# Kernel optimization log

Hardware: AMD Instinct MI355X
Metric: run time of the kernel (lower is better)

## Reference

```python
import jax, jax.numpy as jnp
import numpy as np

ALPHA = 0.2          # LeakyReLU negative slope
NEG = -9e15          # masking value from the torch source


def _gat_multihead(x, adj, W, a):
    """All nheads GATLayers (concat=True math, elu applied by caller).
    x: [B,N,F], adj: [B,N,N], W: [H,F,O], a: [H,2O]. Returns [B,H,N,O].
    Note a_input @ a decomposes as h_i.a[:O] + h_j.a[O:], so we never
    materialize the O(N^2 * 2O) pairwise concat tensor."""
    h = jnp.einsum('bnf,hfo->bhno', x, W)            # [B,H,N,O]
    O = h.shape[-1]
    s1 = jnp.einsum('bhno,ho->bhn', h, a[:, :O])     # h_i . a_src
    s2 = jnp.einsum('bhno,ho->bhn', h, a[:, O:])     # h_j . a_dst
    e = jax.nn.leaky_relu(s1[..., :, None] + s2[..., None, :], ALPHA)  # [B,H,N,N]
    att = jax.nn.softmax(jnp.where(adj[:, None] > 0, e, NEG), axis=-1)
    return jnp.einsum('bhij,bhjo->bhio', att, h)


def _gat_single(x, adj, W, a):
    """out_att GATLayer (concat=False, no elu). W: [F,O], a: [2O]."""
    h = jnp.einsum('bnf,fo->bno', x, W)
    O = W.shape[-1]
    s1 = h @ a[:O]
    s2 = h @ a[O:]
    e = jax.nn.leaky_relu(s1[:, :, None] + s2[:, None, :], ALPHA)
    att = jax.nn.softmax(jnp.where(adj > 0, e, NEG), axis=-1)
    return jnp.einsum('bij,bjo->bio', att, h)


def setup_inputs() -> dict:
    key = jax.random.key(0)
    ks = jax.random.split(key, 10)
    B, N, F = 2, 2048, 768
    H, O = 8, 256
    x = jax.random.normal(ks[0], (B, N, F), dtype=jnp.float32)
    # sparse-ish binary adjacency (adj>0 is all that matters) + self loops
    adj = (jax.random.uniform(ks[1], (B, N, N)) < 0.05).astype(jnp.float32)
    adj = jnp.maximum(adj, jnp.eye(N, dtype=jnp.float32)[None])
    mask = jnp.ones((B, N, 1), dtype=jnp.float32)  # unused by GAT.forward
    s = 0.05
    W_heads = jax.random.normal(ks[2], (H, F, O), dtype=jnp.float32) * s
    a_heads = jax.random.normal(ks[3], (H, 2 * O), dtype=jnp.float32) * s
    W_out = jax.random.normal(ks[4], (H * O, O), dtype=jnp.float32) * s
    a_out = jax.random.normal(ks[5], (2 * O,), dtype=jnp.float32) * s
    W_lin = jax.random.normal(ks[6], (O, H * O), dtype=jnp.float32) * s  # nn.Linear weight [out,in]
    b_lin = jnp.zeros((O,), dtype=jnp.float32)
    W_ln = jax.random.normal(ks[7], (O, O), dtype=jnp.float32) * s
    b_ln = jnp.zeros((O,), dtype=jnp.float32)
    return {"x": x, "adj": adj, "mask": mask, "W_heads": W_heads,
            "a_heads": a_heads, "W_out": W_out, "a_out": a_out,
            "W_lin": W_lin, "b_lin": b_lin, "W_ln": W_ln, "b_ln": b_ln}


def reference(x, adj, mask, W_heads, a_heads, W_out, a_out, W_lin, b_lin, W_ln, b_ln):
    # layer 0: multi-head GAT, elu, concat over heads (dropout=0 in eval)
    hp = jax.nn.elu(_gat_multihead(x, adj, W_heads, a_heads))  # [B,H,N,O]
    B, H, N, O = hp.shape
    x1 = jnp.transpose(hp, (0, 2, 1, 3)).reshape(B, N, H * O)
    # layer 1: residual linear + out_att (concat=False)
    x2 = x1 @ W_lin.T + b_lin + _gat_single(x1, adj, W_out, a_out)
    # final: relu(ln(x))
    return jax.nn.relu(x2 @ W_ln.T + b_ln)
```

## Files before the change

kernel.cpp:

```cpp
#include <hip/hip_runtime.h>
#include <hip/hip_bf16.h>

constexpr int Bb = 2, Nn = 2048, Ff = 768, Hh = 8, Oo = 256;

typedef __attribute__((ext_vector_type(8)))  short   short8;
typedef __attribute__((ext_vector_type(16))) float   f32x16;
typedef __attribute__((ext_vector_type(4)))  unsigned short ushort4_t;

__device__ inline unsigned short f2bf(float f) {
    unsigned u = __float_as_uint(f);
    u = (u + 0x7FFFu + ((u >> 16) & 1u)) >> 16;
    return (unsigned short)u;
}

__device__ inline void wfrag_kn_body(
        const float* __restrict__ W, unsigned short* __restrict__ out,
        int K, int N, int fblk, int t) {
    int f = fblk * 4 + (t >> 6);
    int slot = t & 63, kh = slot >> 5, lm = slot & 31;
    int nfk = K >> 4;
    int nt = f / nfk, kt = f - nt * nfk;
    const float* wp = W + (size_t)(kt * 16 + kh * 8) * N + nt * 32 + lm;
    ushort4_t o0, o1;
    o0.x = f2bf(wp[0]);             o0.y = f2bf(wp[(size_t)N]);
    o0.z = f2bf(wp[2 * (size_t)N]); o0.w = f2bf(wp[3 * (size_t)N]);
    o1.x = f2bf(wp[4 * (size_t)N]); o1.y = f2bf(wp[5 * (size_t)N]);
    o1.z = f2bf(wp[6 * (size_t)N]); o1.w = f2bf(wp[7 * (size_t)N]);
    unsigned short* op = out + (size_t)f * 512 + slot * 8;
    *(ushort4_t*)op = o0;
    *(ushort4_t*)(op + 4) = o1;
}

__device__ inline void wfrag_nk_body(
        const float* __restrict__ W, unsigned short* __restrict__ out,
        int K, int fblk, int t) {
    int f = fblk * 4 + (t >> 6);
    int slot = t & 63, kh = slot >> 5, lm = slot & 31;
    int nfk = K >> 4;
    int nt = f / nfk, kt = f - nt * nfk;
    const float* wp = W + (size_t)(nt * 32 + lm) * K + kt * 16 + kh * 8;
    float4 a = *(const float4*)wp, b = *(const float4*)(wp + 4);
    ushort4_t o0, o1;
    o0.x = f2bf(a.x); o0.y = f2bf(a.y); o0.z = f2bf(a.z); o0.w = f2bf(a.w);
    o1.x = f2bf(b.x); o1.y = f2bf(b.y); o1.z = f2bf(b.z); o1.w = f2bf(b.w);
    unsigned short* op = out + (size_t)f * 512 + slot * 8;
    *(ushort4_t*)op = o0;
    *(ushort4_t*)(op + 4) = o1;
}

__global__ __launch_bounds__(256) void prep_misc_kernel(
        const float* __restrict__ adj, unsigned long long* __restrict__ bits,
        const float* __restrict__ x, unsigned short* __restrict__ x_bf,
        const float* __restrict__ W_heads, unsigned short* __restrict__ WhF,
        const float* __restrict__ W_out,   unsigned short* __restrict__ WoF,
        const float* __restrict__ W_lin,   unsigned short* __restrict__ WlF,
        const float* __restrict__ W_ln,    unsigned short* __restrict__ WnF) {
    int blk = blockIdx.x, t = threadIdx.x;
    if (blk < 32768) {
        size_t gid = (size_t)blk * 256 + t;
        float v = adj[gid];
        unsigned long long m = __ballot(v > 0.f);
        if ((t & 63) == 0) bits[gid >> 6] = m;
    } else if (blk < 35840) {
        size_t i = (size_t)(blk - 32768) * 256 + t;
        float4 v = ((const float4*)x)[i];
        ushort4_t o;
        o.x = f2bf(v.x); o.y = f2bf(v.y); o.z = f2bf(v.z); o.w = f2bf(v.w);
        ((ushort4_t*)x_bf)[i] = o;
    } else if (blk < 36608) {
        int idx = blk - 35840;
        int head = idx / 96, fblk = idx - head * 96;
        wfrag_kn_body(W_heads + (size_t)head * Ff * Oo, WhF + (size_t)head * 384 * 512,
                      Ff, Oo, fblk, t);
    } else if (blk < 36864) {
        wfrag_kn_body(W_out, WoF, Hh * Oo, Oo, blk - 36608, t);
    } else if (blk < 37120) {
        wfrag_nk_body(W_lin, WlF, Hh * Oo, blk - 36864, t);
    } else {
        wfrag_nk_body(W_ln, WnF, Oo, blk - 37120, t);
    }
}

template<int SWAPZ>
__global__ __launch_bounds__(256) void gemm32_kernel(
        const unsigned short* __restrict__ A, int K, long long sA, int bAshift,
        const unsigned short* __restrict__ BF, long long sB, int bmask,
        float* __restrict__ C, long long sC,
        unsigned short* __restrict__ CF, long long sCF, int Mtot,
        const float* __restrict__ bias, int mode,
        const float* __restrict__ aall, int amask,
        float* __restrict__ E1p, float* __restrict__ E1n, float2* __restrict__ E2pn) {
    int z  = SWAPZ ? blockIdx.x : blockIdx.z;
    int mx = SWAPZ ? blockIdx.y : blockIdx.x;
    A  += (size_t)(z >> bAshift) * sA;
    BF += (size_t)(z & bmask) * sB;
    if (C) C += (size_t)z * sC;
    if (CF) CF += (size_t)z * sCF;
    int m0 = mx * 32;
    int t = threadIdx.x;
    int wv = t >> 6, lane = t & 63;
    int lm = lane & 31, kh = lane >> 5;
    int nfk = K >> 4;
    __shared__ __align__(16) unsigned short As[32][136];
    f32x16 acc[2] = {};
    int sr = t >> 3, sc2 = (t & 7) * 16;
    const unsigned short* ag  = A + (size_t)(m0 + sr) * K + sc2;
    const unsigned short* bg0 = BF + (size_t)(wv * 2) * nfk * 512;
    const unsigned short* bg1 = bg0 + (size_t)nfk * 512;
    for (int k0 = 0; k0 < K; k0 += 128) {
        *(short8*)&As[sr][sc2]     = *(const short8*)(ag + k0);
        *(short8*)&As[sr][sc2 + 8] = *(const short8*)(ag + k0 + 8);
        int kt0 = k0 >> 4;
        __syncthreads();
#pragma unroll
        for (int s = 0; s < 8; ++s) {
            short8 a0 = *(const short8*)&As[lm][s * 16 + kh * 8];
            short8 b0 = *(const short8*)(bg0 + (size_t)(kt0 + s) * 512 + lane * 8);
            short8 b1 = *(const short8*)(bg1 + (size_t)(kt0 + s) * 512 + lane * 8);
            acc[0] = __builtin_amdgcn_mfma_f32_32x32x16_bf16(a0, b0, acc[0], 0, 0, 0);
            acc[1] = __builtin_amdgcn_mfma_f32_32x32x16_bf16(a0, b1, acc[1], 0, 0, 0);
        }
        __syncthreads();
    }
#pragma unroll
    for (int nt = 0; nt < 2; ++nt) {
        int colg = wv * 64 + nt * 32 + lm;
        float bv = (mode == 2) ? bias[colg] : 0.f;
        if (C) {
#pragma unroll
            for (int reg = 0; reg < 16; ++reg) {
                int rl = 4 * kh + (reg & 3) + 8 * (reg >> 2);
                float v = acc[nt][reg];
                if (mode == 2) { v += bv; v = fmaxf(v, 0.f); }
                C[(size_t)(m0 + rl) * 256 + colg] = v;
            }
        }
        if (mode == 1) {
#pragma unroll
            for (int q = 0; q < 4; ++q) {
                int kt = m0 / 16 + (q >> 1);
                size_t fi = ((size_t)(colg >> 5) * (Mtot / 16) + kt) * 512 +
                            ((q & 1) * 32 + (colg & 31)) * 8 + kh * 4;
                ushort4_t pk;
                pk.x = f2bf(acc[nt][q * 4 + 0]);
                pk.y = f2bf(acc[nt][q * 4 + 1]);
                pk.z = f2bf(acc[nt][q * 4 + 2]);
                pk.w = f2bf(acc[nt][q * 4 + 3]);
                *(ushort4_t*)(CF + fi) = pk;
            }
        }
    }
    if (aall) {
        const float* av = aall + (size_t)(z & amask) * 512;
        float a1v0 = av[wv * 64 + lm],       a1v1 = av[wv * 64 + 32 + lm];
        float a2v0 = av[256 + wv * 64 + lm], a2v1 = av[256 + wv * 64 + 32 + lm];
        float* sbuf = (float*)As;
#pragma unroll
        for (int reg = 0; reg < 16; ++reg) {
            int rl = 4 * kh + (reg & 3) + 8 * (reg >> 2);
            float v1 = acc[0][reg] * a1v0 + acc[1][reg] * a1v1;
            float v2 = acc[0][reg] * a2v0 + acc[1][reg] * a2v1;
#pragma unroll
            for (int m = 1; m <= 16; m <<= 1) {
                v1 += __shfl_xor(v1, m, 64);
                v2 += __shfl_xor(v2, m, 64);
            }
            if (lm == 0) { sbuf[rl * 8 + wv] = v1; sbuf[rl * 8 + 4 + wv] = v2; }
        }
        __syncthreads();
        if (t < 32) {
            float s1 = sbuf[t * 8] + sbuf[t * 8 + 1] + sbuf[t * 8 + 2] + sbuf[t * 8 + 3];
            float s2 = sbuf[t * 8 + 4] + sbuf[t * 8 + 5] + sbuf[t * 8 + 6] + sbuf[t * 8 + 7];
            size_t ei = (size_t)z * Nn + m0 + t;
            E1p[ei] = __expf(s1);
            E1n[ei] = __expf(0.2f * s1);
            E2pn[ei] = make_float2(__expf(s2), __expf(0.2f * s2));
        }
    }
}

__global__ __launch_bounds__(512) void gemm32_dual_kernel(
        const unsigned short* __restrict__ A, int K, long long sA,
        const unsigned short* __restrict__ BF,
        unsigned short* __restrict__ h2f, float* __restrict__ lin,
        const float* __restrict__ a_out,
        float* __restrict__ E1p, float* __restrict__ E1n, float2* __restrict__ E2pn) {
    int b = blockIdx.z, ng = blockIdx.y;
    A += (size_t)b * sA;
    int nfk = K >> 4;
    BF += (size_t)ng * 8 * nfk * 512;
    int m0 = blockIdx.x * 32;
    int t = threadIdx.x;
    int wv = t >> 6, lane = t & 63;
    int lm = lane & 31, kh = lane >> 5;
    __shared__ __align__(16) unsigned short As[32][136];
    f32x16 acc = {};
    int sr = t >> 4, sc2 = (t & 15) * 8;
    const unsigned short* ag = A + (size_t)(m0 + sr) * K + sc2;
    const unsigned short* bg = BF + (size_t)wv * nfk * 512;
    for (int k0 = 0; k0 < K; k0 += 128) {
        *(short8*)&As[sr][sc2] = *(const short8*)(ag + k0);
        int kt0 = k0 >> 4;
        __syncthreads();
#pragma unroll
        for (int s = 0; s < 8; ++s) {
            short8 a0 = *(const short8*)&As[lm][s * 16 + kh * 8];
            short8 b0 = *(const short8*)(bg + (size_t)(kt0 + s) * 512 + lane * 8);
            acc = __builtin_amdgcn_mfma_f32_32x32x16_bf16(a0, b0, acc, 0, 0, 0);
        }
        __syncthreads();
    }
    int colg = wv * 32 + lm;
    if (ng == 1) {
        float* C = lin + (size_t)b * Nn * 256;
#pragma unroll
        for (int reg = 0; reg < 16; ++reg) {
            int rl = 4 * kh + (reg & 3) + 8 * (reg >> 2);
            C[(size_t)(m0 + rl) * 256 + colg] = acc[reg];
        }
    } else {
        unsigned short* CF = h2f + (size_t)b * 524288;
#pragma unroll
        for (int q = 0; q < 4; ++q) {
            int kt = m0 / 16 + (q >> 1);
            size_t fi = ((size_t)(colg >> 5) * 128 + kt) * 512 +
                        ((q & 1) * 32 + (colg & 31)) * 8 + kh * 4;
            ushort4_t pk;
            pk.x = f2bf(acc[q * 4 + 0]);
            pk.y = f2bf(acc[q * 4 + 1]);
            pk.z = f2bf(acc[q * 4 + 2]);
            pk.w = f2bf(acc[q * 4 + 3]);
            *(ushort4_t*)(CF + fi) = pk;
        }
        float a1v = a_out[colg];
        float a2v = a_out[256 + colg];
        float* sbuf = (float*)As;
#pragma unroll
        for (int reg = 0; reg < 16; ++reg) {
            int rl = 4 * kh + (reg & 3) + 8 * (reg >> 2);
            float v1 = acc[reg] * a1v;
            float v2 = acc[reg] * a2v;
#pragma unroll
            for (int m = 1; m <= 16; m <<= 1) {
                v1 += __shfl_xor(v1, m, 64);
                v2 += __shfl_xor(v2, m, 64);
            }
            if (lm == 0) { sbuf[rl * 16 + wv] = v1; sbuf[rl * 16 + 8 + wv] = v2; }
        }
        __syncthreads();
        if (t < 32) {
            float s1 = 0.f, s2 = 0.f;
#pragma unroll
            for (int k = 0; k < 8; ++k) {
                s1 += sbuf[t * 16 + k];
                s2 += sbuf[t * 16 + 8 + k];
            }
            size_t ei = (size_t)b * Nn + m0 + t;
            E1p[ei] = __expf(s1);
            E1n[ei] = __expf(0.2f * s1);
            E2pn[ei] = make_float2(__expf(s2), __expf(0.2f * s2));
        }
    }
}

__global__ __launch_bounds__(256) void gemm32_final_kernel(
        const float* __restrict__ pacc, const float* __restrict__ plsum,
        const float* __restrict__ lin, const float* __restrict__ b_lin,
        const unsigned short* __restrict__ BF, const float* __restrict__ b_ln,
        float* __restrict__ out) {
    int b = blockIdx.z, oc = blockIdx.y;
    int m0 = blockIdx.x * 32;
    int t = threadIdx.x;
    int wv = t >> 6, lane = t & 63;
    int lm = lane & 31, kh = lane >> 5;
    constexpr int nfk = 16;
    __shared__ __align__(16) unsigned short As[32][136];
    f32x16 acc = {};
    int sr = t >> 3, sc2 = (t & 7) * 16;
    int row = m0 + sr;
    int BN = Bb * Nn;
    size_t prow = (size_t)b * Nn + row;
    float li = 1.f / (plsum[prow] + plsum[prow + BN] + plsum[prow + 2 * BN] + plsum[prow + 3 * BN]);
    size_t ps4 = (size_t)Bb * Nn * 256;
    const unsigned short* bg = BF + (size_t)(oc * 4 + wv) * nfk * 512;
    for (int k0 = 0; k0 < 256; k0 += 128) {
        int o = k0 + sc2;
        size_t pidx = prow * 256 + o;
#pragma unroll
        for (int g = 0; g < 4; ++g) {
            float4 s4 = *(const float4*)(pacc + pidx + 4 * g);
#pragma unroll
            for (int k = 1; k < 4; ++k) {
                float4 q = *(const float4*)(pacc + k * ps4 + pidx + 4 * g);
                s4.x += q.x; s4.y += q.y; s4.z += q.z; s4.w += q.w;
            }
            float4 lv = *(const float4*)(lin + pidx + 4 * g);
            float4 bv = *(const float4*)(b_lin + o + 4 * g);
            ushort4_t pk;
            pk.x = f2bf(s4.x * li + lv.x + bv.x);
            pk.y = f2bf(s4.y * li + lv.y + bv.y);
            pk.z = f2bf(s4.z * li + lv.z + bv.z);
            pk.w = f2bf(s4.w * li + lv.w + bv.w);
            *(ushort4_t*)&As[sr][sc2 + 4 * g] = pk;
        }
        int kt0 = k0 >> 4;
        __syncthreads();
#pragma unroll
        for (int s = 0; s < 8; ++s) {
            short8 a0 = *(const short8*)&As[lm][s * 16 + kh * 8];
            short8 b0 = *(const short8*)(bg + (size_t)(kt0 + s) * 512 + lane * 8);
            acc = __builtin_amdgcn_mfma_f32_32x32x16_bf16(a0, b0, acc, 0, 0, 0);
        }
        __syncthreads();
    }
    float* C = out + (size_t)b * Nn * 256;
    int colg = oc * 128 + wv * 32 + lm;
    float bv = b_ln[colg];
#pragma unroll
    for (int reg = 0; reg < 16; ++reg) {
        int rl = 4 * kh + (reg & 3) + 8 * (reg >> 2);
        float v = fmaxf(acc[reg] + bv, 0.f);
        C[(size_t)(m0 + rl) * 256 + colg] = v;
    }
}

template<int JLEN, int MODE, int SWAPXY>
__global__ __launch_bounds__(256, 4) void attn32_kernel(
        const unsigned short* __restrict__ hfrag,
        const unsigned* __restrict__ bits,
        const float* __restrict__ E1p, const float* __restrict__ E1n,
        const float2* __restrict__ E2pn,
        unsigned short* __restrict__ outbf, int ldo,
        float* __restrict__ pacc, float* __restrict__ plsum,
        int hshift) {
    constexpr int W = JLEN / 32, NC = JLEN / 64, ABS = W + 1;
    int it = SWAPXY ? blockIdx.y : blockIdx.x;
    int bh = SWAPXY ? blockIdx.x : blockIdx.y;
    int js = blockIdx.z;
    int b = bh >> hshift, hd = bh & ((1 << hshift) - 1);
    int i0 = it * 32, jbase = js * JLEN;
    int kt0 = js * (JLEN / 16);
    int t = threadIdx.x, lane = t & 63;
    int wv = t >> 6, lm = lane & 31, kh = lane >> 5;
    int ti = t & 31, jq = t >> 5;

    __shared__ unsigned ab[32 * ABS];
    __shared__ __align__(16) unsigned short ps[2][32][64];
    __shared__ float lred[32][9];
    __shared__ float linv[32];

    const unsigned* bb = bits + ((size_t)b * Nn + i0) * 64 + (jbase >> 5);
    for (int k = t; k < 32 * W; k += 256) {
        int r = k / W, w0 = k - r * W;
        ab[r * ABS + w0] = bb[(size_t)r * 64 + w0];
    }
    __syncthreads();

    float e1p = E1p[(size_t)bh * Nn + i0 + ti];
    float e1n = E1n[(size_t)bh * Nn + i0 + ti];
    const float4* e2base = (const float4*)(E2pn + (size_t)bh * Nn + jbase);

    const unsigned short* bg0 = hfrag + (size_t)bh * 524288 + (size_t)(wv * 2) * 128 * 512;
    const unsigned short* bg1 = bg0 + 128 * 512;

    f32x16 acc[2] = {};
    float lp0 = 0.f, lp1 = 0.f;
    short8 Bpp[4][2];

    auto loadBs = [&](int c, int s, int slot) {
        int kt = kt0 + c * 4 + s;
        Bpp[slot][0] = *(const short8*)(bg0 + (size_t)kt * 512 + lane * 8);
        Bpp[slot][1] = *(const short8*)(bg1 + (size_t)kt * 512 + lane * 8);
    };
    auto computeP = [&](int c, int buf) {
        int cj = c * 64;
        unsigned word = ab[ti * ABS + (cj >> 5) + (jq >> 2)];
        unsigned field = (word >> ((jq & 3) * 8)) & 0xffu;
        const float4* ep = e2base + ((cj + jq * 8) >> 1);
        unsigned pk[4];
#pragma unroll
        for (int u = 0; u < 4; ++u) {
            float4 q = ep[u];
            float p0 = fmaxf(e1p * q.x, e1n * q.y);
            p0 = ((field >> (2 * u)) & 1u) ? p0 : 0.f;
            float p1 = fmaxf(e1p * q.z, e1n * q.w);
            p1 = ((field >> (2 * u + 1)) & 1u) ? p1 : 0.f;
            if (u & 1) lp1 += p0 + p1; else lp0 += p0 + p1;
            __hip_bfloat162 hv = __float22bfloat162_rn(make_float2(p0, p1));
            pk[u] = *(unsigned*)&hv;
        }
        uint4 v; v.x = pk[0]; v.y = pk[1]; v.z = pk[2]; v.w = pk[3];
        *(uint4*)&ps[buf][ti][(jq ^ (ti & 7)) * 8] = v;
    };
    auto mfmaS = [&](int buf, int s, int slot) {
        int g = 2 * s + kh;
        short8 a0 = *(const short8*)&ps[buf][lm][(g ^ (lm & 7)) * 8];
        __builtin_amdgcn_s_setprio(1);
        acc[0] = __builtin_amdgcn_mfma_f32_32x32x16_bf16(a0, Bpp[slot][0], acc[0], 0, 0, 0);
        acc[1] = __builtin_amdgcn_mfma_f32_32x32x16_bf16(a0, Bpp[slot][1], acc[1], 0, 0, 0);
        __builtin_amdgcn_s_setprio(0);
    };

    computeP(0, 0);
    loadBs(0, 0, 0); loadBs(0, 1, 1); loadBs(0, 2, 2); loadBs(0, 3, 3);
    __syncthreads();
    for (int c = 0; c + 1 < NC; ++c) {
        int cb = c & 1, nb = cb ^ 1;
        computeP(c + 1, nb);
        mfmaS(cb, 0, 0);  loadBs(c + 1, 0, 0);
        mfmaS(cb, 1, 1);  loadBs(c + 1, 1, 1);
        mfmaS(cb, 2, 2);  loadBs(c + 1, 2, 2);
        mfmaS(cb, 3, 3);  loadBs(c + 1, 3, 3);
        __syncthreads();
    }
    {
        int cb = (NC - 1) & 1;
        mfmaS(cb, 0, 0);
        mfmaS(cb, 1, 1);
        mfmaS(cb, 2, 2);
        mfmaS(cb, 3, 3);
    }

    lred[ti][jq] = lp0 + lp1;
    __syncthreads();
    if (MODE == 0) {
        if (t < 32) {
            float s = 0.f;
#pragma unroll
            for (int k = 0; k < 8; ++k) s += lred[t][k];
            linv[t] = 1.f / s;
        }
        __syncthreads();
#pragma unroll
        for (int nt = 0; nt < 2; ++nt) {
            int o = wv * 64 + nt * 32 + lm;
#pragma unroll
            for (int reg = 0; reg < 16; ++reg) {
                int rl = 4 * kh + (reg & 3) + 8 * (reg >> 2);
                float v = acc[nt][reg] * linv[rl];
                v = v > 0.f ? v : expm1f(v);
                outbf[((size_t)b * Nn + i0 + rl) * ldo + (size_t)hd * Oo + o] = f2bf(v);
            }
        }
    } else {
        if (t < 32) {
            float s = 0.f;
#pragma unroll
            for (int k = 0; k < 8; ++k) s += lred[t][k];
            plsum[((size_t)js * Bb + b) * Nn + i0 + t] = s;
        }
        float* pa = pacc + (((size_t)js * Bb + b) * Nn) * 256;
#pragma unroll
        for (int nt = 0; nt < 2; ++nt) {
            int o = wv * 64 + nt * 32 + lm;
#pragma unroll
            for (int reg = 0; reg < 16; ++reg) {
                int rl = 4 * kh + (reg & 3) + 8 * (reg >> 2);
                pa[(size_t)(i0 + rl) * 256 + o] = acc[nt][reg];
            }
        }
    }
}

template<int JLEN, int MODE, int SWAPXY>
__global__ __launch_bounds__(256, 2) void attn64_kernel(
        const unsigned short* __restrict__ hfrag,
        const unsigned* __restrict__ bits,
        const float* __restrict__ E1p, const float* __restrict__ E1n,
        const float2* __restrict__ E2pn,
        unsigned short* __restrict__ outbf, int ldo,
        float* __restrict__ pacc, float* __restrict__ plsum,
        int hshift) {
    constexpr int W = JLEN / 32, NC = JLEN / 64, ABS = W + 1;
    int it = SWAPXY ? blockIdx.y : blockIdx.x;
    int bh = SWAPXY ? blockIdx.x : blockIdx.y;
    int js = blockIdx.z;
    int b = bh >> hshift, hd = bh & ((1 << hshift) - 1);
    int i0 = it * 64, jbase = js * JLEN;
    int kt0 = js * (JLEN / 16);
    int t = threadIdx.x, lane = t & 63;
    int wv = t >> 6, lm = lane & 31, kh = lane >> 5;
    int ti = t & 31, jq = t >> 5;

    __shared__ unsigned ab[64 * ABS];
    __shared__ __align__(16) unsigned short ps[2][64][64];
    __shared__ float lred[64][9];
    __shared__ float linv[64];

    const unsigned* bb = bits + ((size_t)b * Nn + i0) * 64 + (jbase >> 5);
    for (int k = t; k < 64 * W; k += 256) {
        int r = k / W, w0 = k - r * W;
        ab[r * ABS + w0] = bb[(size_t)r * 64 + w0];
    }
    __syncthreads();

    float e1pA = E1p[(size_t)bh * Nn + i0 + ti];
    float e1nA = E1n[(size_t)bh * Nn + i0 + ti];
    float e1pB = E1p[(size_t)bh * Nn + i0 + 32 + ti];
    float e1nB = E1n[(size_t)bh * Nn + i0 + 32 + ti];
    const float4* e2base = (const float4*)(E2pn + (size_t)bh * Nn + jbase);

    const unsigned short* bg0 = hfrag + (size_t)bh * 524288 + (size_t)(wv * 2) * 128 * 512;
    const unsigned short* bg1 = bg0 + 128 * 512;

    f32x16 acc[4] = {};
    float lpA = 0.f, lpB = 0.f;
    short8 Bpp[4][2];

    auto loadBs = [&](int c, int s, int slot) {
        int kt = kt0 + c * 4 + s;
        Bpp[slot][0] = *(const short8*)(bg0 + (size_t)kt * 512 + lane * 8);
        Bpp[slot][1] = *(const short8*)(bg1 + (size_t)kt * 512 + lane * 8);
    };
    auto computeP = [&](int c, int buf) {
        int cj = c * 64;
        int wi = (cj >> 5) + (jq >> 2);
        unsigned wordA = ab[ti * ABS + wi];
        unsigned wordB = ab[(ti + 32) * ABS + wi];
        unsigned fieldA = (wordA >> ((jq & 3) * 8)) & 0xffu;
        unsigned fieldB = (wordB >> ((jq & 3) * 8)) & 0xffu;
        const float4* ep = e2base + ((cj + jq * 8) >> 1);
        unsigned pkA[4], pkB[4];
#pragma unroll
        for (int u = 0; u < 4; ++u) {
            float4 q = ep[u];
            float a0v = fmaxf(e1pA * q.x, e1nA * q.y);
            a0v = ((fieldA >> (2 * u)) & 1u) ? a0v : 0.f;
            float a1v = fmaxf(e1pA * q.z, e1nA * q.w);
            a1v = ((fieldA >> (2 * u + 1)) & 1u) ? a1v : 0.f;
            lpA += a0v + a1v;
            float b0v = fmaxf(e1pB * q.x, e1nB * q.y);
            b0v = ((fieldB >> (2 * u)) & 1u) ? b0v : 0.f;
            float b1v = fmaxf(e1pB * q.z, e1nB * q.w);
            b1v = ((fieldB >> (2 * u + 1)) & 1u) ? b1v : 0.f;
            lpB += b0v + b1v;
            __hip_bfloat162 hA = __float22bfloat162_rn(make_float2(a0v, a1v));
            __hip_bfloat162 hB = __float22bfloat162_rn(make_float2(b0v, b1v));
            pkA[u] = *(unsigned*)&hA;
            pkB[u] = *(unsigned*)&hB;
        }
        int col = (jq ^ (ti & 7)) * 8;
        uint4 vA; vA.x = pkA[0]; vA.y = pkA[1]; vA.z = pkA[2]; vA.w = pkA[3];
        uint4 vB; vB.x = pkB[0]; vB.y = pkB[1]; vB.z = pkB[2]; vB.w = pkB[3];
        *(uint4*)&ps[buf][ti][col] = vA;
        *(uint4*)&ps[buf][ti + 32][col] = vB;
    };
    auto mfmaS = [&](int buf, int s, int slot) {
        int g = 2 * s + kh;
        int col = (g ^ (lm & 7)) * 8;
        short8 a0 = *(const short8*)&ps[buf][lm][col];
        short8 a1 = *(const short8*)&ps[buf][32 + lm][col];
        __builtin_amdgcn_s_setprio(1);
        acc[0] = __builtin_amdgcn_mfma_f32_32x32x16_bf16(a0, Bpp[slot][0], acc[0], 0, 0, 0);
        acc[1] = __builtin_amdgcn_mfma_f32_32x32x16_bf16(a0, Bpp[slot][1], acc[1], 0, 0, 0);
        acc[2] = __builtin_amdgcn_mfma_f32_32x32x16_bf16(a1, Bpp[slot][0], acc[2], 0, 0, 0);
        acc[3] = __builtin_amdgcn_mfma_f32_32x32x16_bf16(a1, Bpp[slot][1], acc[3], 0, 0, 0);
        __builtin_amdgcn_s_setprio(0);
    };

    computeP(0, 0);
    loadBs(0, 0, 0); loadBs(0, 1, 1); loadBs(0, 2, 2); loadBs(0, 3, 3);
    __syncthreads();
    for (int c = 0; c + 1 < NC; ++c) {
        int cb = c & 1, nb = cb ^ 1;
        computeP(c + 1, nb);
        mfmaS(cb, 0, 0);  loadBs(c + 1, 0, 0);
        mfmaS(cb, 1, 1);  loadBs(c + 1, 1, 1);
        mfmaS(cb, 2, 2);  loadBs(c + 1, 2, 2);
        mfmaS(cb, 3, 3);  loadBs(c + 1, 3, 3);
        __syncthreads();
    }
    {
        int cb = (NC - 1) & 1;
        mfmaS(cb, 0, 0);
        mfmaS(cb, 1, 1);
        mfmaS(cb, 2, 2);
        mfmaS(cb, 3, 3);
    }

    lred[ti][jq] = lpA;
    lred[ti + 32][jq] = lpB;
    __syncthreads();
    if (MODE == 0) {
        if (t < 64) {
            float s = 0.f;
#pragma unroll
            for (int k = 0; k < 8; ++k) s += lred[t][k];
            linv[t] = 1.f / s;
        }
        __syncthreads();
#pragma unroll
        for (int ih = 0; ih < 2; ++ih) {
#pragma unroll
            for (int nt = 0; nt < 2; ++nt) {
                int o = wv * 64 + nt * 32 + lm;
#pragma unroll
                for (int reg = 0; reg < 16; ++reg) {
                    int rl = 4 * kh + (reg & 3) + 8 * (reg >> 2);
                    int row = ih * 32 + rl;
                    float v = acc[ih * 2 + nt][reg] * linv[row];
                    v = v > 0.f ? v : expm1f(v);
                    outbf[((size_t)b * Nn + i0 + row) * ldo + (size_t)hd * Oo + o] = f2bf(v);
                }
            }
        }
    } else {
        if (t < 64) {
            float s = 0.f;
#pragma unroll
            for (int k = 0; k < 8; ++k) s += lred[t][k];
            plsum[((size_t)js * Bb + b) * Nn + i0 + t] = s;
        }
        float* pa = pacc + (((size_t)js * Bb + b) * Nn) * 256;
#pragma unroll
        for (int ih = 0; ih < 2; ++ih) {
#pragma unroll
            for (int nt = 0; nt < 2; ++nt) {
                int o = wv * 64 + nt * 32 + lm;
#pragma unroll
                for (int reg = 0; reg < 16; ++reg) {
                    int rl = 4 * kh + (reg & 3) + 8 * (reg >> 2);
                    int row = ih * 32 + rl;
                    pa[(size_t)(i0 + row) * 256 + o] = acc[ih * 2 + nt][reg];
                }
            }
        }
    }
}

extern "C" void kernel_launch(void* const* d_in, const int* in_sizes, int n_in,
                              void* d_out, int out_size, void* d_ws, size_t ws_size,
                              hipStream_t stream) {
    const float* x       = (const float*)d_in[0];
    const float* adj     = (const float*)d_in[1];
    const float* W_heads = (const float*)d_in[3];
    const float* a_heads = (const float*)d_in[4];
    const float* W_out   = (const float*)d_in[5];
    const float* a_out   = (const float*)d_in[6];
    const float* W_lin   = (const float*)d_in[7];
    const float* b_lin   = (const float*)d_in[8];
    const float* W_ln    = (const float*)d_in[9];
    const float* b_ln    = (const float*)d_in[10];

    char* w = (char*)d_ws;
    float* pacc     = (float*)(w);
    float* lin      = (float*)(w + 33554432);
    float* E1p_mh   = (float*)(w + 41943040);
    float* E1n_mh   = (float*)(w + 42074112);
    float2* E2pn_mh = (float2*)(w + 42205184);
    float* E1p_sh   = (float*)(w + 42467328);
    float* E1n_sh   = (float*)(w + 42483712);
    float2* E2pn_sh = (float2*)(w + 42500096);
    unsigned long long* bits = (unsigned long long*)(w + 42532864);
    unsigned short* x_bf  = (unsigned short*)(w + 43581440);
    unsigned short* WhF   = (unsigned short*)(w + 49872896);
    unsigned short* WoF   = (unsigned short*)(w + 53018624);
    unsigned short* WlF   = (unsigned short*)(w + 54067200);
    unsigned short* WnF   = (unsigned short*)(w + 55115776);
    unsigned short* hfrag = (unsigned short*)(w + 55246848);
    unsigned short* h2frag= (unsigned short*)(w + 72024064);
    unsigned short* x1_bf = (unsigned short*)(w + 74121216);
    float* plsum = E1p_mh;

    prep_misc_kernel<<<37152, 256, 0, stream>>>(
        adj, bits, x, x_bf, W_heads, WhF, W_out, WoF, W_lin, WlF, W_ln, WnF);

    gemm32_kernel<1><<<dim3(Bb * Hh, Nn / 32, 1), 256, 0, stream>>>(
        x_bf, Ff, (long long)Nn * Ff, 3, WhF, 384LL * 512, 7,
        nullptr, 0, hfrag, 524288, Nn, nullptr, 1,
        a_heads, 7, E1p_mh, E1n_mh, E2pn_mh);
    attn64_kernel<2048, 0, 1><<<dim3(Bb * Hh, Nn / 64, 1), 256, 0, stream>>>(
        hfrag, (const unsigned*)bits, E1p_mh, E1n_mh, E2pn_mh,
        x1_bf, Hh * Oo, nullptr, nullptr, 3);
    gemm32_dual_kernel<<<dim3(Nn / 32, 2, Bb), 512, 0, stream>>>(
        x1_bf, Hh * Oo, (long long)Nn * Hh * Oo, WoF, h2frag, lin,
        a_out, E1p_sh, E1n_sh, E2pn_sh);
    attn32_kernel<512, 1, 0><<<dim3(Nn / 32, Bb, 4), 256, 0, stream>>>(
        h2frag, (const unsigned*)bits, E1p_sh, E1n_sh, E2pn_sh,
        nullptr, 0, pacc, plsum, 0);
    gemm32_final_kernel<<<dim3(Nn / 32, 2, Bb), 256, 0, stream>>>(
        pacc, plsum, lin, b_lin, WnF, b_ln, (float*)d_out);
}
```

Measured before the change: 237.0 us.

## Widen head GEMM to 64-row tiles and split second attention eightfold

```diff
diff --git a/kernel.cpp b/kernel.cpp
--- a/kernel.cpp
+++ b/kernel.cpp
@@ -2,6 +2,7 @@
 #include <hip/hip_bf16.h>
 
 constexpr int Bb = 2, Nn = 2048, Ff = 768, Hh = 8, Oo = 256;
+constexpr int NSPLIT = 8;
 
 typedef __attribute__((ext_vector_type(8)))  short   short8;
 typedef __attribute__((ext_vector_type(16))) float   f32x16;
@@ -81,101 +82,95 @@
     }
 }
 
-template<int SWAPZ>
-__global__ __launch_bounds__(256) void gemm32_kernel(
+__global__ __launch_bounds__(256) void gemm64_kernel(
         const unsigned short* __restrict__ A, int K, long long sA, int bAshift,
         const unsigned short* __restrict__ BF, long long sB, int bmask,
-        float* __restrict__ C, long long sC,
         unsigned short* __restrict__ CF, long long sCF, int Mtot,
-        const float* __restrict__ bias, int mode,
         const float* __restrict__ aall, int amask,
         float* __restrict__ E1p, float* __restrict__ E1n, float2* __restrict__ E2pn) {
-    int z  = SWAPZ ? blockIdx.x : blockIdx.z;
-    int mx = SWAPZ ? blockIdx.y : blockIdx.x;
+    int z  = blockIdx.x;
+    int mx = blockIdx.y;
     A  += (size_t)(z >> bAshift) * sA;
     BF += (size_t)(z & bmask) * sB;
-    if (C) C += (size_t)z * sC;
-    if (CF) CF += (size_t)z * sCF;
-    int m0 = mx * 32;
+    CF += (size_t)z * sCF;
+    int m0 = mx * 64;
     int t = threadIdx.x;
     int wv = t >> 6, lane = t & 63;
     int lm = lane & 31, kh = lane >> 5;
     int nfk = K >> 4;
-    __shared__ __align__(16) unsigned short As[32][136];
-    f32x16 acc[2] = {};
-    int sr = t >> 3, sc2 = (t & 7) * 16;
+    __shared__ __align__(16) unsigned short As[64][136];
+    f32x16 acc[4] = {};
+    int sr = t >> 2, sc2 = (t & 3) * 32;
     const unsigned short* ag  = A + (size_t)(m0 + sr) * K + sc2;
     const unsigned short* bg0 = BF + (size_t)(wv * 2) * nfk * 512;
     const unsigned short* bg1 = bg0 + (size_t)nfk * 512;
     for (int k0 = 0; k0 < K; k0 += 128) {
-        *(short8*)&As[sr][sc2]     = *(const short8*)(ag + k0);
-        *(short8*)&As[sr][sc2 + 8] = *(const short8*)(ag + k0 + 8);
+        *(short8*)&As[sr][sc2]      = *(const short8*)(ag + k0);
+        *(short8*)&As[sr][sc2 + 8]  = *(const short8*)(ag + k0 + 8);
+        *(short8*)&As[sr][sc2 + 16] = *(const short8*)(ag + k0 + 16);
+        *(short8*)&As[sr][sc2 + 24] = *(const short8*)(ag + k0 + 24);
         int kt0 = k0 >> 4;
         __syncthreads();
 #pragma unroll
         for (int s = 0; s < 8; ++s) {
             short8 a0 = *(const short8*)&As[lm][s * 16 + kh * 8];
+            short8 a1 = *(const short8*)&As[32 + lm][s * 16 + kh * 8];
             short8 b0 = *(const short8*)(bg0 + (size_t)(kt0 + s) * 512 + lane * 8);
             short8 b1 = *(const short8*)(bg1 + (size_t)(kt0 + s) * 512 + lane * 8);
             acc[0] = __builtin_amdgcn_mfma_f32_32x32x16_bf16(a0, b0, acc[0], 0, 0, 0);
             acc[1] = __builtin_amdgcn_mfma_f32_32x32x16_bf16(a0, b1, acc[1], 0, 0, 0);
-        }
-        __syncthreads();
-    }
-#pragma unroll
-    for (int nt = 0; nt < 2; ++nt) {
-        int colg = wv * 64 + nt * 32 + lm;
-        float bv = (mode == 2) ? bias[colg] : 0.f;
-        if (C) {
-#pragma unroll
-            for (int reg = 0; reg < 16; ++reg) {
-                int rl = 4 * kh + (reg & 3) + 8 * (reg >> 2);
-                float v = acc[nt][reg];
-                if (mode == 2) { v += bv; v = fmaxf(v, 0.f); }
-                C[(size_t)(m0 + rl) * 256 + colg] = v;
-            }
-        }
-        if (mode == 1) {
+            acc[2] = __builtin_amdgcn_mfma_f32_32x32x16_bf16(a1, b0, acc[2], 0, 0, 0);
+            acc[3] = __builtin_amdgcn_mfma_f32_32x32x16_bf16(a1, b1, acc[3], 0, 0, 0);
+        }
+        __syncthreads();
+    }
+#pragma unroll
+    for (int hf = 0; hf < 2; ++hf) {
+#pragma unroll
+        for (int nt = 0; nt < 2; ++nt) {
+            int colg = wv * 64 + nt * 32 + lm;
 #pragma unroll
             for (int q = 0; q < 4; ++q) {
-                int kt = m0 / 16 + (q >> 1);
+                int kt = m0 / 16 + hf * 2 + (q >> 1);
                 size_t fi = ((size_t)(colg >> 5) * (Mtot / 16) + kt) * 512 +
                             ((q & 1) * 32 + (colg & 31)) * 8 + kh * 4;
                 ushort4_t pk;
-                pk.x = f2bf(acc[nt][q * 4 + 0]);
-                pk.y = f2bf(acc[nt][q * 4 + 1]);
-                pk.z = f2bf(acc[nt][q * 4 + 2]);
-                pk.w = f2bf(acc[nt][q * 4 + 3]);
+                pk.x = f2bf(acc[hf * 2 + nt][q * 4 + 0]);
+                pk.y = f2bf(acc[hf * 2 + nt][q * 4 + 1]);
+                pk.z = f2bf(acc[hf * 2 + nt][q * 4 + 2]);
+                pk.w = f2bf(acc[hf * 2 + nt][q * 4 + 3]);
                 *(ushort4_t*)(CF + fi) = pk;
             }
         }
     }
-    if (aall) {
-        const float* av = aall + (size_t)(z & amask) * 512;
-        float a1v0 = av[wv * 64 + lm],       a1v1 = av[wv * 64 + 32 + lm];
-        float a2v0 = av[256 + wv * 64 + lm], a2v1 = av[256 + wv * 64 + 32 + lm];
-        float* sbuf = (float*)As;
+    const float* av = aall + (size_t)(z & amask) * 512;
+    float a1v0 = av[wv * 64 + lm],       a1v1 = av[wv * 64 + 32 + lm];
+    float a2v0 = av[256 + wv * 64 + lm], a2v1 = av[256 + wv * 64 + 32 + lm];
+    float* sbuf = (float*)As;
+#pragma unroll
+    for (int hf = 0; hf < 2; ++hf) {
 #pragma unroll
         for (int reg = 0; reg < 16; ++reg) {
             int rl = 4 * kh + (reg & 3) + 8 * (reg >> 2);
-            float v1 = acc[0][reg] * a1v0 + acc[1][reg] * a1v1;
-            float v2 = acc[0][reg] * a2v0 + acc[1][reg] * a2v1;
+            float v1 = acc[hf * 2 + 0][reg] * a1v0 + acc[hf * 2 + 1][reg] * a1v1;
+            float v2 = acc[hf * 2 + 0][reg] * a2v0 + acc[hf * 2 + 1][reg] * a2v1;
 #pragma unroll
             for (int m = 1; m <= 16; m <<= 1) {
                 v1 += __shfl_xor(v1, m, 64);
                 v2 += __shfl_xor(v2, m, 64);
             }
-            if (lm == 0) { sbuf[rl * 8 + wv] = v1; sbuf[rl * 8 + 4 + wv] = v2; }
-        }
-        __syncthreads();
-        if (t < 32) {
-            float s1 = sbuf[t * 8] + sbuf[t * 8 + 1] + sbuf[t * 8 + 2] + sbuf[t * 8 + 3];
-            float s2 = sbuf[t * 8 + 4] + sbuf[t * 8 + 5] + sbuf[t * 8 + 6] + sbuf[t * 8 + 7];
-            size_t ei = (size_t)z * Nn + m0 + t;
-            E1p[ei] = __expf(s1);
-            E1n[ei] = __expf(0.2f * s1);
-            E2pn[ei] = make_float2(__expf(s2), __expf(0.2f * s2));
-        }
+            int row = hf * 32 + rl;
+            if (lm == 0) { sbuf[row * 8 + wv] = v1; sbuf[row * 8 + 4 + wv] = v2; }
+        }
+    }
+    __syncthreads();
+    if (t < 64) {
+        float s1 = sbuf[t * 8] + sbuf[t * 8 + 1] + sbuf[t * 8 + 2] + sbuf[t * 8 + 3];
+        float s2 = sbuf[t * 8 + 4] + sbuf[t * 8 + 5] + sbuf[t * 8 + 6] + sbuf[t * 8 + 7];
+        size_t ei = (size_t)z * Nn + m0 + t;
+        E1p[ei] = __expf(s1);
+        E1n[ei] = __expf(0.2f * s1);
+        E2pn[ei] = make_float2(__expf(s2), __expf(0.2f * s2));
     }
 }
 
@@ -280,7 +275,10 @@
     int row = m0 + sr;
     int BN = Bb * Nn;
     size_t prow = (size_t)b * Nn + row;
-    float li = 1.f / (plsum[prow] + plsum[prow + BN] + plsum[prow + 2 * BN] + plsum[prow + 3 * BN]);
+    float ls = 0.f;
+#pragma unroll
+    for (int k = 0; k < NSPLIT; ++k) ls += plsum[prow + k * BN];
+    float li = 1.f / ls;
     size_t ps4 = (size_t)Bb * Nn * 256;
     const unsigned short* bg = BF + (size_t)(oc * 4 + wv) * nfk * 512;
     for (int k0 = 0; k0 < 256; k0 += 128) {
@@ -290,7 +288,7 @@
         for (int g = 0; g < 4; ++g) {
             float4 s4 = *(const float4*)(pacc + pidx + 4 * g);
 #pragma unroll
-            for (int k = 1; k < 4; ++k) {
+            for (int k = 1; k < NSPLIT; ++k) {
                 float4 q = *(const float4*)(pacc + k * ps4 + pidx + 4 * g);
                 s4.x += q.x; s4.y += q.y; s4.z += q.z; s4.w += q.w;
             }
@@ -665,9 +663,9 @@
     prep_misc_kernel<<<37152, 256, 0, stream>>>(
         adj, bits, x, x_bf, W_heads, WhF, W_out, WoF, W_lin, WlF, W_ln, WnF);
 
-    gemm32_kernel<1><<<dim3(Bb * Hh, Nn / 32, 1), 256, 0, stream>>>(
+    gemm64_kernel<<<dim3(Bb * Hh, Nn / 64, 1), 256, 0, stream>>>(
         x_bf, Ff, (long long)Nn * Ff, 3, WhF, 384LL * 512, 7,
-        nullptr, 0, hfrag, 524288, Nn, nullptr, 1,
+        hfrag, 524288, Nn,
         a_heads, 7, E1p_mh, E1n_mh, E2pn_mh);
     attn64_kernel<2048, 0, 1><<<dim3(Bb * Hh, Nn / 64, 1), 256, 0, stream>>>(
         hfrag, (const unsigned*)bits, E1p_mh, E1n_mh, E2pn_mh,
@@ -675,7 +673,7 @@
     gemm32_dual_kernel<<<dim3(Nn / 32, 2, Bb), 512, 0, stream>>>(
         x1_bf, Hh * Oo, (long long)Nn * Hh * Oo, WoF, h2frag, lin,
         a_out, E1p_sh, E1n_sh, E2pn_sh);
-    attn32_kernel<512, 1, 0><<<dim3(Nn / 32, Bb, 4), 256, 0, stream>>>(
+    attn32_kernel<256, 1, 0><<<dim3(Nn / 32, Bb, NSPLIT), 256, 0, stream>>>(
         h2frag, (const unsigned*)bits, E1p_sh, E1n_sh, E2pn_sh,
         nullptr, 0, pacc, plsum, 0);
     gemm32_final_kernel<<<dim3(Nn / 32, 2, Bb), 256, 0, stream>>>(
```

Result: slower. 248.9 us (+5.0%).
